# Performance work log

Measured on AMD Instinct MI355X. Metric: run time of the kernel, lower is better.

The kernel has to match this reference:

```python
import jax, jax.numpy as jnp
import numpy as np

D_MODEL = 512
N_HEADS = 8
D_HEAD = D_MODEL // N_HEADS
SCALE = D_HEAD ** -0.5


def _rel_shift(x):
    # x: (b, h, qlen, klen) -> Transformer-XL relative shift
    b, h, qlen, klen = x.shape
    x = jnp.pad(x, ((0, 0), (0, 0), (0, 0), (1, 0)))        # (b,h,q,k+1)
    x = x.reshape(b, h, klen + 1, qlen)
    x = x[:, :, 1:, :].reshape(b, h, qlen, klen)
    return x


def setup_inputs() -> dict:
    key = jax.random.key(0)
    ks = jax.random.split(key, 12)
    B, S = 2, 2048
    P = 2 * S - 1
    w = lambda k, shape: (jax.random.normal(k, shape, jnp.float32) * 0.02)
    return {
        "x": jax.random.normal(ks[0], (B, S, D_MODEL), jnp.float32),
        "pos_emb": jax.random.normal(ks[1], (P, D_MODEL), jnp.float32),
        "Wq": w(ks[2], (D_MODEL, D_MODEL)), "bq": jnp.zeros((D_MODEL,), jnp.float32),
        "Wk": w(ks[3], (D_MODEL, D_MODEL)), "bk": jnp.zeros((D_MODEL,), jnp.float32),
        "Wv": w(ks[4], (D_MODEL, D_MODEL)), "bv": jnp.zeros((D_MODEL,), jnp.float32),
        "Wp": w(ks[5], (D_MODEL, D_MODEL)),
        "Wo": w(ks[6], (D_MODEL, D_MODEL)), "bo": jnp.zeros((D_MODEL,), jnp.float32),
        "pos_bias_u": w(ks[7], (N_HEADS, D_HEAD)),
        "pos_bias_v": w(ks[8], (N_HEADS, D_HEAD)),
    }


def reference(x, pos_emb, Wq, bq, Wk, bk, Wv, bv, Wp, Wo, bo, pos_bias_u, pos_bias_v):
    B, S, _ = x.shape
    # projections (torch Linear: y = x @ W^T + b; here W stored as (in, out))
    q = (x @ Wq + bq).reshape(B, S, N_HEADS, D_HEAD)
    k = (x @ Wk + bk).reshape(B, S, N_HEADS, D_HEAD)
    v = (x @ Wv + bv).reshape(B, S, N_HEADS, D_HEAD)
    p = (pos_emb @ Wp).reshape(-1, N_HEADS, D_HEAD)  # (2S-1, H, D)

    # content score: (q + u) @ k^T  -> (B,H,S,S)
    content = jnp.einsum("bshd,bthd->bhst", q + pos_bias_u, k)
    # position score: (q + v_bias) @ p^T -> (B,H,S,2S-1), then rel_shift
    pos = jnp.einsum("bshd,phd->bhsp", q + pos_bias_v, p)
    pos = _rel_shift(pos)[..., :S]  # trim to kv_len

    attn = jax.nn.softmax((content + pos) * SCALE, axis=-1)
    out = jnp.einsum("bhst,bthd->bshd", attn, v).reshape(B, S, D_MODEL)
    out = out @ Wo + bo
    return out
```

## Files before the change

kernel.cpp:

```cpp
#include <hip/hip_runtime.h>

#define DM    512
#define NH    8
#define DH    64
#define SEQ   2048
#define PLEN  4095
#define NB    2
#define ATT_SCALE 0.125f

typedef __attribute__((ext_vector_type(8))) _Float16 half8;
typedef __attribute__((ext_vector_type(4))) float   floatx4;

__global__ __launch_bounds__(256)
void prep(const float* __restrict__ x, const float* __restrict__ pe,
          const float* __restrict__ W0, const float* __restrict__ W1,
          const float* __restrict__ W2, const float* __restrict__ W3,
          const float* __restrict__ W4,
          _Float16* __restrict__ x16, _Float16* __restrict__ pe16,
          _Float16* __restrict__ Wt)
{
    __shared__ _Float16 tile[64 * 72];
    const int z = blockIdx.z;
    const int t = threadIdx.x;

    if (z < 2) {
        const float* src = z ? pe : x;
        _Float16* dst = z ? pe16 : x16;
        const long n = z ? (long)PLEN * DM : (long)NB * SEQ * DM;
        const long i = ((long)blockIdx.x * 256 + t) * 8;
        if (i >= n) return;
        float4 f0 = *(const float4*)(src + i);
        float4 f1 = *(const float4*)(src + i + 4);
        half8 o;
        o[0] = (_Float16)f0.x; o[1] = (_Float16)f0.y;
        o[2] = (_Float16)f0.z; o[3] = (_Float16)f0.w;
        o[4] = (_Float16)f1.x; o[5] = (_Float16)f1.y;
        o[6] = (_Float16)f1.z; o[7] = (_Float16)f1.w;
        *(half8*)(dst + i) = o;
        return;
    }
    if (blockIdx.x >= 64) return;
    const int wz = z - 2;
    const float* W = (wz == 0) ? W0 : (wz == 1) ? W1 : (wz == 2) ? W2
                   : (wz == 3) ? W3 : W4;
    _Float16* dst_base = Wt + (size_t)wz * DM * DM;
    const int n0 = (blockIdx.x & 7) * 64, k0 = (blockIdx.x >> 3) * 64;
    {
        const int kr = t >> 2, nch = (t & 3) * 16;
        const float* src = W + (size_t)(k0 + kr) * DM + n0 + nch;
        float4 f0 = *(const float4*)(src + 0);
        float4 f1 = *(const float4*)(src + 4);
        float4 f2 = *(const float4*)(src + 8);
        float4 f3 = *(const float4*)(src + 12);
        _Float16* trow = &tile[kr * 72 + nch];
        trow[0]  = (_Float16)f0.x; trow[1]  = (_Float16)f0.y;
        trow[2]  = (_Float16)f0.z; trow[3]  = (_Float16)f0.w;
        trow[4]  = (_Float16)f1.x; trow[5]  = (_Float16)f1.y;
        trow[6]  = (_Float16)f1.z; trow[7]  = (_Float16)f1.w;
        trow[8]  = (_Float16)f2.x; trow[9]  = (_Float16)f2.y;
        trow[10] = (_Float16)f2.z; trow[11] = (_Float16)f2.w;
        trow[12] = (_Float16)f3.x; trow[13] = (_Float16)f3.y;
        trow[14] = (_Float16)f3.z; trow[15] = (_Float16)f3.w;
    }
    __syncthreads();
    {
        const int nr = t >> 2, kch = (t & 3) * 16;
        half8 o0, o1;
#pragma unroll
        for (int i = 0; i < 8; ++i) o0[i] = tile[(kch + i) * 72 + nr];
#pragma unroll
        for (int i = 0; i < 8; ++i) o1[i] = tile[(kch + 8 + i) * 72 + nr];
        _Float16* dst = dst_base + (size_t)(n0 + nr) * DM + k0 + kch;
        *(half8*)dst = o0;
        *(half8*)(dst + 8) = o1;
    }
}

__global__ __launch_bounds__(256)
void gemm_qkvp(const _Float16* __restrict__ X, const _Float16* __restrict__ Pe,
               const _Float16* __restrict__ Wt,
               const float* __restrict__ bq, const float* __restrict__ bk,
               const float* __restrict__ bv, const float* __restrict__ bu,
               const float* __restrict__ bvb,
               _Float16* __restrict__ qu16, _Float16* __restrict__ qv16,
               _Float16* __restrict__ k16, _Float16* __restrict__ vt16,
               _Float16* __restrict__ p16)
{
    __shared__ _Float16 aS[64 * 72];
    __shared__ _Float16 wS[64 * 72];

    const int t = threadIdx.x;
    const int w = t >> 6, lane = t & 63, quad = lane >> 4, l16 = lane & 15;
    const int z = blockIdx.z;
    const int n0 = blockIdx.x * 64;
    const int m0 = blockIdx.y * 64;
    const int srow = t >> 2, sch = (t & 3) * 16;
    const _Float16* A = (z == 3) ? Pe : X;
    const _Float16* Wz = Wt + (size_t)z * DM * DM;

    int arow = m0 + srow;
    if (z == 3 && arow > PLEN - 1) arow = PLEN - 1;
    const _Float16* arowp = A + (size_t)arow * DM + sch;
    const _Float16* wrowp = Wz + (size_t)(n0 + srow) * DM + sch;

    floatx4 acc[4];
#pragma unroll
    for (int ct = 0; ct < 4; ++ct) acc[ct] = (floatx4){0.f, 0.f, 0.f, 0.f};

    half8 pa0 = *(const half8*)arowp;
    half8 pa1 = *(const half8*)(arowp + 8);
    half8 pw0 = *(const half8*)wrowp;
    half8 pw1 = *(const half8*)(wrowp + 8);

    for (int k0 = 0; k0 < DM; k0 += 64) {
        __syncthreads();
        *(half8*)&aS[srow * 72 + sch]     = pa0;
        *(half8*)&aS[srow * 72 + sch + 8] = pa1;
        *(half8*)&wS[srow * 72 + sch]     = pw0;
        *(half8*)&wS[srow * 72 + sch + 8] = pw1;
        __syncthreads();
        if (k0 + 64 < DM) {
            pa0 = *(const half8*)(arowp + k0 + 64);
            pa1 = *(const half8*)(arowp + k0 + 72);
            pw0 = *(const half8*)(wrowp + k0 + 64);
            pw1 = *(const half8*)(wrowp + k0 + 72);
        }
#pragma unroll
        for (int kb = 0; kb < 2; ++kb) {
            half8 af = *(const half8*)&aS[(16 * w + l16) * 72 + kb * 32 + quad * 8];
#pragma unroll
            for (int ct = 0; ct < 4; ++ct) {
                half8 bf = *(const half8*)&wS[(16 * ct + l16) * 72 + kb * 32 + quad * 8];
                acc[ct] = __builtin_amdgcn_mfma_f32_16x16x32_f16(af, bf, acc[ct], 0, 0, 0);
            }
        }
    }

    const int h = n0 >> 6;
    if (z == 0) {
#pragma unroll
        for (int ct = 0; ct < 4; ++ct) {
            const int n = n0 + 16 * ct + l16;
            const float bval = bq[n], uval = bu[n], vval = bvb[n];
#pragma unroll
            for (int r = 0; r < 4; ++r) {
                const int m = m0 + 16 * w + 4 * quad + r;
                const int b = m >> 11, s = m & 2047;
                const size_t dst = ((size_t)((h * NB + b) * SEQ) + s) * DH + (n & 63);
                const float q = acc[ct][r] + bval;
                qu16[dst] = (_Float16)((q + uval) * ATT_SCALE);
                qv16[dst] = (_Float16)((q + vval) * ATT_SCALE);
            }
        }
    } else if (z == 1) {
#pragma unroll
        for (int ct = 0; ct < 4; ++ct) {
            const int n = n0 + 16 * ct + l16;
            const float bval = bk[n];
#pragma unroll
            for (int r = 0; r < 4; ++r) {
                const int m = m0 + 16 * w + 4 * quad + r;
                const int b = m >> 11, s = m & 2047;
                k16[((size_t)((h * NB + b) * SEQ) + s) * DH + (n & 63)] =
                    (_Float16)(acc[ct][r] + bval);
            }
        }
    } else if (z == 2) {
        __syncthreads();
#pragma unroll
        for (int ct = 0; ct < 4; ++ct) {
            const float bval = bv[n0 + 16 * ct + l16];
#pragma unroll
            for (int r = 0; r < 4; ++r)
                aS[(16 * w + 4 * quad + r) * 72 + 16 * ct + l16] =
                    (_Float16)(acc[ct][r] + bval);
        }
        __syncthreads();
        const int b = m0 >> 11, s0 = m0 & 2047;
        const int drow = t >> 2;
        half8 o0, o1;
#pragma unroll
        for (int i = 0; i < 8; ++i) o0[i] = aS[(sch + i) * 72 + drow];
#pragma unroll
        for (int i = 0; i < 8; ++i) o1[i] = aS[(sch + 8 + i) * 72 + drow];
        _Float16* dst = vt16 + ((size_t)((h * NB + b) * DH) + drow) * SEQ + s0 + sch;
        *(half8*)dst = o0;
        *(half8*)(dst + 8) = o1;
    } else {
#pragma unroll
        for (int ct = 0; ct < 4; ++ct) {
            const int n = n0 + 16 * ct + l16;
#pragma unroll
            for (int r = 0; r < 4; ++r) {
                const int m = m0 + 16 * w + 4 * quad + r;
                if (m < PLEN)
                    p16[((size_t)h * PLEN + m) * DH + (n & 63)] = (_Float16)acc[ct][r];
            }
        }
    }
}

__global__ __launch_bounds__(256, 2)
void relattn_mfma(const _Float16* __restrict__ QU,
                  const _Float16* __restrict__ QV,
                  const _Float16* __restrict__ Kp,
                  const _Float16* __restrict__ VT,
                  const _Float16* __restrict__ Pp,
                  _Float16* __restrict__ Out)
{
    __shared__ _Float16 kS[64 * 72];
    __shared__ _Float16 pS[128 * 72];
    __shared__ _Float16 vS[64 * 72];
    __shared__ _Float16 tS[64 * 88];

    const int t = threadIdx.x;
    const int w = t >> 6, lane = t & 63, quad = lane >> 4, l16 = lane & 15;
    const int i0 = blockIdx.x * 64;
    const int h = blockIdx.y, b = blockIdx.z;
    const size_t hb = (size_t)(h * NB + b);
    const int cbase = 48 - 16 * w;

    half8 qa[2], va[2];
    {
        const _Float16* qrow = QU + (hb * SEQ + i0 + 16 * w + l16) * DH + quad * 8;
        const _Float16* vrow = QV + (hb * SEQ + i0 + 16 * w + l16) * DH + quad * 8;
        qa[0] = *(const half8*)qrow;       qa[1] = *(const half8*)(qrow + 32);
        va[0] = *(const half8*)vrow;       va[1] = *(const half8*)(vrow + 32);
    }

    floatx4 O[4];
    float lsum[4] = {0.f, 0.f, 0.f, 0.f};
#pragma unroll
    for (int ct = 0; ct < 4; ++ct) O[ct] = (floatx4){0.f, 0.f, 0.f, 0.f};

    const int srow = t >> 2, schunk = (t & 3) * 16;
    const int prow = t >> 1, pch = (t & 1) * 32;

    const _Float16* Kbase = Kp + hb * SEQ * DH;
    const _Float16* Vbase = VT + hb * DH * SEQ;
    const _Float16* Pbase = Pp + (size_t)h * PLEN * DH;
    const int rbase0 = (SEQ - 1) - i0 - 63;

    half8 pk0, pk1, pv0, pv1;
    half8 pp0 = {}, pp1 = {}, pp2 = {}, pp3 = {};
    {
        const _Float16* src = Kbase + (size_t)srow * DH + schunk;
        pk0 = *(const half8*)src;
        pk1 = *(const half8*)(src + 8);
        const _Float16* vsrc = Vbase + (size_t)srow * SEQ + schunk;
        pv0 = *(const half8*)vsrc;
        pv1 = *(const half8*)(vsrc + 8);
        if (prow < 127) {
            const _Float16* psrc = Pbase + (size_t)(rbase0 + prow) * DH + pch;
            pp0 = *(const half8*)(psrc + 0);
            pp1 = *(const half8*)(psrc + 8);
            pp2 = *(const half8*)(psrc + 16);
            pp3 = *(const half8*)(psrc + 24);
        }
    }

    for (int j0 = 0; j0 < SEQ; j0 += 64) {
        __syncthreads();

        *(half8*)&kS[srow * 72 + schunk]     = pk0;
        *(half8*)&kS[srow * 72 + schunk + 8] = pk1;
        *(half8*)&vS[srow * 72 + schunk]     = pv0;
        *(half8*)&vS[srow * 72 + schunk + 8] = pv1;
        if (prow < 127) {
            *(half8*)&pS[prow * 72 + pch + 0]  = pp0;
            *(half8*)&pS[prow * 72 + pch + 8]  = pp1;
            *(half8*)&pS[prow * 72 + pch + 16] = pp2;
            *(half8*)&pS[prow * 72 + pch + 24] = pp3;
        }
        __syncthreads();

        if (j0 + 64 < SEQ) {
            const _Float16* src = Kbase + (size_t)(j0 + 64 + srow) * DH + schunk;
            pk0 = *(const half8*)src;
            pk1 = *(const half8*)(src + 8);
            const _Float16* vsrc = Vbase + (size_t)srow * SEQ + j0 + 64 + schunk;
            pv0 = *(const half8*)vsrc;
            pv1 = *(const half8*)(vsrc + 8);
            if (prow < 127) {
                const _Float16* psrc = Pbase + (size_t)(rbase0 + j0 + 64 + prow) * DH + pch;
                pp0 = *(const half8*)(psrc + 0);
                pp1 = *(const half8*)(psrc + 8);
                pp2 = *(const half8*)(psrc + 16);
                pp3 = *(const half8*)(psrc + 24);
            }
        }

        {
            floatx4 Tacc[5];
#pragma unroll
            for (int c2 = 0; c2 < 5; ++c2) Tacc[c2] = (floatx4){0.f, 0.f, 0.f, 0.f};
#pragma unroll
            for (int kb = 0; kb < 2; ++kb) {
#pragma unroll
                for (int c2 = 0; c2 < 5; ++c2) {
                    half8 bf = *(const half8*)&pS[(cbase + 16 * c2 + l16) * 72 + kb * 32 + quad * 8];
                    Tacc[c2] = __builtin_amdgcn_mfma_f32_16x16x32_f16(va[kb], bf, Tacc[c2], 0, 0, 0);
                }
            }
#pragma unroll
            for (int c2 = 0; c2 < 5; ++c2)
#pragma unroll
                for (int r = 0; r < 4; ++r)
                    tS[(16 * w + 4 * quad + r) * 88 + 16 * c2 + l16] = (_Float16)Tacc[c2][r];
        }
        asm volatile("" ::: "memory");

        floatx4 Sc[4];
#pragma unroll
        for (int ct = 0; ct < 4; ++ct) Sc[ct] = (floatx4){0.f, 0.f, 0.f, 0.f};
#pragma unroll
        for (int kb = 0; kb < 2; ++kb) {
#pragma unroll
            for (int ct = 0; ct < 4; ++ct) {
                half8 bf = *(const half8*)&kS[(16 * ct + l16) * 72 + kb * 32 + quad * 8];
                Sc[ct] = __builtin_amdgcn_mfma_f32_16x16x32_f16(qa[kb], bf, Sc[ct], 0, 0, 0);
            }
        }
#pragma unroll
        for (int ct = 0; ct < 4; ++ct)
#pragma unroll
            for (int r = 0; r < 4; ++r) {
                const int il16 = 4 * quad + r;
                const int c = 16 * ct + l16 - il16 + 15;
                const float e = __expf(Sc[ct][r] +
                                       (float)tS[(16 * w + il16) * 88 + c]);
                Sc[ct][r] = e;
                lsum[r] += e;
            }
        asm volatile("" ::: "memory");

#pragma unroll
        for (int ct = 0; ct < 4; ++ct)
#pragma unroll
            for (int r = 0; r < 4; ++r)
                tS[(16 * w + 4 * quad + r) * 88 + 16 * ct + l16] = (_Float16)Sc[ct][r];
        asm volatile("" ::: "memory");

#pragma unroll
        for (int kb = 0; kb < 2; ++kb) {
            half8 af = *(const half8*)&tS[(16 * w + l16) * 88 + kb * 32 + quad * 8];
#pragma unroll
            for (int ct = 0; ct < 4; ++ct) {
                half8 bf = *(const half8*)&vS[(16 * ct + l16) * 72 + kb * 32 + quad * 8];
                O[ct] = __builtin_amdgcn_mfma_f32_16x16x32_f16(af, bf, O[ct], 0, 0, 0);
            }
        }
        asm volatile("" ::: "memory");
    }

#pragma unroll
    for (int r = 0; r < 4; ++r) {
#pragma unroll
        for (int m = 1; m < 16; m <<= 1) lsum[r] += __shfl_xor(lsum[r], m);
        const float inv = 1.f / lsum[r];
        _Float16* orow = Out + (size_t)(b * SEQ + i0 + 16 * w + 4 * quad + r) * DM + h * DH;
#pragma unroll
        for (int ct = 0; ct < 4; ++ct)
            orow[16 * ct + l16] = (_Float16)(O[ct][r] * inv);
    }
}

__global__ __launch_bounds__(256)
void gemm_out(const _Float16* __restrict__ A, const _Float16* __restrict__ Wt,
              const float* __restrict__ bias, float* __restrict__ Out)
{
    __shared__ _Float16 aS[64 * 72];
    __shared__ _Float16 wS[64 * 72];

    const int t = threadIdx.x;
    const int w = t >> 6, lane = t & 63, quad = lane >> 4, l16 = lane & 15;
    const int n0 = blockIdx.x * 64;
    const int m0 = blockIdx.y * 64;
    const int srow = t >> 2, sch = (t & 3) * 16;

    const _Float16* arowp = A + (size_t)(m0 + srow) * DM + sch;
    const _Float16* wrowp = Wt + (size_t)(n0 + srow) * DM + sch;

    floatx4 acc[4];
#pragma unroll
    for (int ct = 0; ct < 4; ++ct) acc[ct] = (floatx4){0.f, 0.f, 0.f, 0.f};

    half8 pa0 = *(const half8*)arowp;
    half8 pa1 = *(const half8*)(arowp + 8);
    half8 pw0 = *(const half8*)wrowp;
    half8 pw1 = *(const half8*)(wrowp + 8);

    for (int k0 = 0; k0 < DM; k0 += 64) {
        __syncthreads();
        *(half8*)&aS[srow * 72 + sch]     = pa0;
        *(half8*)&aS[srow * 72 + sch + 8] = pa1;
        *(half8*)&wS[srow * 72 + sch]     = pw0;
        *(half8*)&wS[srow * 72 + sch + 8] = pw1;
        __syncthreads();
        if (k0 + 64 < DM) {
            pa0 = *(const half8*)(arowp + k0 + 64);
            pa1 = *(const half8*)(arowp + k0 + 72);
            pw0 = *(const half8*)(wrowp + k0 + 64);
            pw1 = *(const half8*)(wrowp + k0 + 72);
        }
#pragma unroll
        for (int kb = 0; kb < 2; ++kb) {
            half8 af = *(const half8*)&aS[(16 * w + l16) * 72 + kb * 32 + quad * 8];
#pragma unroll
            for (int ct = 0; ct < 4; ++ct) {
                half8 bf = *(const half8*)&wS[(16 * ct + l16) * 72 + kb * 32 + quad * 8];
                acc[ct] = __builtin_amdgcn_mfma_f32_16x16x32_f16(af, bf, acc[ct], 0, 0, 0);
            }
        }
    }

#pragma unroll
    for (int ct = 0; ct < 4; ++ct) {
        const int n = n0 + 16 * ct + l16;
        const float bval = bias[n];
#pragma unroll
        for (int r = 0; r < 4; ++r) {
            const int m = m0 + 16 * w + 4 * quad + r;
            Out[(size_t)m * DM + n] = acc[ct][r] + bval;
        }
    }
}

extern "C" void kernel_launch(void* const* d_in, const int* in_sizes, int n_in,
                              void* d_out, int out_size, void* d_ws, size_t ws_size,
                              hipStream_t stream)
{
    (void)in_sizes; (void)n_in; (void)out_size; (void)ws_size;
    const float* x   = (const float*)d_in[0];
    const float* pe  = (const float*)d_in[1];
    const float* Wq  = (const float*)d_in[2];
    const float* bq  = (const float*)d_in[3];
    const float* Wk  = (const float*)d_in[4];
    const float* bk  = (const float*)d_in[5];
    const float* Wv  = (const float*)d_in[6];
    const float* bv  = (const float*)d_in[7];
    const float* Wp  = (const float*)d_in[8];
    const float* Wo  = (const float*)d_in[9];
    const float* bo  = (const float*)d_in[10];
    const float* pbu = (const float*)d_in[11];
    const float* pbv = (const float*)d_in[12];
    float* out = (float*)d_out;

    const size_t nX  = (size_t)NB * SEQ * DM;
    const size_t nPe = (size_t)PLEN * DM;
    const size_t nW  = (size_t)DM * DM;
    const size_t nH  = (size_t)NH * NB * SEQ * DH;
    const size_t nPh = (size_t)NH * PLEN * DH;

    _Float16* x16  = (_Float16*)d_ws;
    _Float16* pe16 = x16 + nX;
    _Float16* wt   = pe16 + nPe;
    _Float16* qu16 = wt + 5 * nW;
    _Float16* qv16 = qu16 + nH;
    _Float16* k16  = qv16 + nH;
    _Float16* vt16 = k16 + nH;
    _Float16* p16  = vt16 + nH;
    _Float16* ow16 = p16 + nPh;

    dim3 blk(256);
    prep<<<dim3(1024, 1, 7), blk, 0, stream>>>(x, pe, Wq, Wk, Wv, Wp, Wo,
                                               x16, pe16, wt);
    gemm_qkvp<<<dim3(8, 64, 4), blk, 0, stream>>>(x16, pe16, wt,
                                                  bq, bk, bv, pbu, pbv,
                                                  qu16, qv16, k16, vt16, p16);
    relattn_mfma<<<dim3(SEQ / 64, NH, NB), blk, 0, stream>>>(
        qu16, qv16, k16, vt16, p16, ow16);
    gemm_out<<<dim3(8, 64), blk, 0, stream>>>(ow16, wt + 4 * nW, bo, out);
}
```

Before: 187.0 us.

## Fuse fp32-to-fp16 activation conversion into projection GEMM and repad score tile

Removes the separate pass that converts x and pos_emb to fp16 in the prep kernel. The QKVP GEMM now loads fp32 activations directly and converts them while staging into shared memory, saving a full write and re-read of the converted activations. The cost is that each GEMM block reads twice the bytes per A element, and those rows are re-read across the 8 column blocks. The shared score tile row pitch also changes from 88 to 84 halves, which alters the LDS bank access pattern.

After: 202.3 us. 1.08x slower.

```diff
diff --git a/kernel.cpp b/kernel.cpp
--- a/kernel.cpp
+++ b/kernel.cpp
@@ -7,40 +7,19 @@
 #define PLEN  4095
 #define NB    2
 #define ATT_SCALE 0.125f
+#define TP    84
 
 typedef __attribute__((ext_vector_type(8))) _Float16 half8;
 typedef __attribute__((ext_vector_type(4))) float   floatx4;
 
 __global__ __launch_bounds__(256)
-void prep(const float* __restrict__ x, const float* __restrict__ pe,
-          const float* __restrict__ W0, const float* __restrict__ W1,
+void prep(const float* __restrict__ W0, const float* __restrict__ W1,
           const float* __restrict__ W2, const float* __restrict__ W3,
-          const float* __restrict__ W4,
-          _Float16* __restrict__ x16, _Float16* __restrict__ pe16,
-          _Float16* __restrict__ Wt)
+          const float* __restrict__ W4, _Float16* __restrict__ Wt)
 {
     __shared__ _Float16 tile[64 * 72];
-    const int z = blockIdx.z;
     const int t = threadIdx.x;
-
-    if (z < 2) {
-        const float* src = z ? pe : x;
-        _Float16* dst = z ? pe16 : x16;
-        const long n = z ? (long)PLEN * DM : (long)NB * SEQ * DM;
-        const long i = ((long)blockIdx.x * 256 + t) * 8;
-        if (i >= n) return;
-        float4 f0 = *(const float4*)(src + i);
-        float4 f1 = *(const float4*)(src + i + 4);
-        half8 o;
-        o[0] = (_Float16)f0.x; o[1] = (_Float16)f0.y;
-        o[2] = (_Float16)f0.z; o[3] = (_Float16)f0.w;
-        o[4] = (_Float16)f1.x; o[5] = (_Float16)f1.y;
-        o[6] = (_Float16)f1.z; o[7] = (_Float16)f1.w;
-        *(half8*)(dst + i) = o;
-        return;
-    }
-    if (blockIdx.x >= 64) return;
-    const int wz = z - 2;
+    const int wz = blockIdx.z;
     const float* W = (wz == 0) ? W0 : (wz == 1) ? W1 : (wz == 2) ? W2
                    : (wz == 3) ? W3 : W4;
     _Float16* dst_base = Wt + (size_t)wz * DM * DM;
@@ -77,7 +56,7 @@
 }
 
 __global__ __launch_bounds__(256)
-void gemm_qkvp(const _Float16* __restrict__ X, const _Float16* __restrict__ Pe,
+void gemm_qkvp(const float* __restrict__ X, const float* __restrict__ Pe,
                const _Float16* __restrict__ Wt,
                const float* __restrict__ bq, const float* __restrict__ bk,
                const float* __restrict__ bv, const float* __restrict__ bu,
@@ -95,33 +74,48 @@
     const int n0 = blockIdx.x * 64;
     const int m0 = blockIdx.y * 64;
     const int srow = t >> 2, sch = (t & 3) * 16;
-    const _Float16* A = (z == 3) ? Pe : X;
+    const float* A = (z == 3) ? Pe : X;
     const _Float16* Wz = Wt + (size_t)z * DM * DM;
 
     int arow = m0 + srow;
     if (z == 3 && arow > PLEN - 1) arow = PLEN - 1;
-    const _Float16* arowp = A + (size_t)arow * DM + sch;
+    const float* arowp = A + (size_t)arow * DM + sch;
     const _Float16* wrowp = Wz + (size_t)(n0 + srow) * DM + sch;
 
     floatx4 acc[4];
 #pragma unroll
     for (int ct = 0; ct < 4; ++ct) acc[ct] = (floatx4){0.f, 0.f, 0.f, 0.f};
 
-    half8 pa0 = *(const half8*)arowp;
-    half8 pa1 = *(const half8*)(arowp + 8);
+    float4 pa0 = *(const float4*)(arowp + 0);
+    float4 pa1 = *(const float4*)(arowp + 4);
+    float4 pa2 = *(const float4*)(arowp + 8);
+    float4 pa3 = *(const float4*)(arowp + 12);
     half8 pw0 = *(const half8*)wrowp;
     half8 pw1 = *(const half8*)(wrowp + 8);
 
     for (int k0 = 0; k0 < DM; k0 += 64) {
         __syncthreads();
-        *(half8*)&aS[srow * 72 + sch]     = pa0;
-        *(half8*)&aS[srow * 72 + sch + 8] = pa1;
+        {
+            half8 h0, h1;
+            h0[0] = (_Float16)pa0.x; h0[1] = (_Float16)pa0.y;
+            h0[2] = (_Float16)pa0.z; h0[3] = (_Float16)pa0.w;
+            h0[4] = (_Float16)pa1.x; h0[5] = (_Float16)pa1.y;
+            h0[6] = (_Float16)pa1.z; h0[7] = (_Float16)pa1.w;
+            h1[0] = (_Float16)pa2.x; h1[1] = (_Float16)pa2.y;
+            h1[2] = (_Float16)pa2.z; h1[3] = (_Float16)pa2.w;
+            h1[4] = (_Float16)pa3.x; h1[5] = (_Float16)pa3.y;
+            h1[6] = (_Float16)pa3.z; h1[7] = (_Float16)pa3.w;
+            *(half8*)&aS[srow * 72 + sch]     = h0;
+            *(half8*)&aS[srow * 72 + sch + 8] = h1;
+        }
         *(half8*)&wS[srow * 72 + sch]     = pw0;
         *(half8*)&wS[srow * 72 + sch + 8] = pw1;
         __syncthreads();
         if (k0 + 64 < DM) {
-            pa0 = *(const half8*)(arowp + k0 + 64);
-            pa1 = *(const half8*)(arowp + k0 + 72);
+            pa0 = *(const float4*)(arowp + k0 + 64);
+            pa1 = *(const float4*)(arowp + k0 + 68);
+            pa2 = *(const float4*)(arowp + k0 + 72);
+            pa3 = *(const float4*)(arowp + k0 + 76);
             pw0 = *(const half8*)(wrowp + k0 + 64);
             pw1 = *(const half8*)(wrowp + k0 + 72);
         }
@@ -211,7 +205,7 @@
     __shared__ _Float16 kS[64 * 72];
     __shared__ _Float16 pS[128 * 72];
     __shared__ _Float16 vS[64 * 72];
-    __shared__ _Float16 tS[64 * 88];
+    __shared__ _Float16 tS[64 * TP];
 
     const int t = threadIdx.x;
     const int w = t >> 6, lane = t & 63, quad = lane >> 4, l16 = lane & 15;
@@ -306,7 +300,7 @@
             for (int c2 = 0; c2 < 5; ++c2)
 #pragma unroll
                 for (int r = 0; r < 4; ++r)
-                    tS[(16 * w + 4 * quad + r) * 88 + 16 * c2 + l16] = (_Float16)Tacc[c2][r];
+                    tS[(16 * w + 4 * quad + r) * TP + 16 * c2 + l16] = (_Float16)Tacc[c2][r];
         }
         asm volatile("" ::: "memory");
 
@@ -328,7 +322,7 @@
                 const int il16 = 4 * quad + r;
                 const int c = 16 * ct + l16 - il16 + 15;
                 const float e = __expf(Sc[ct][r] +
-                                       (float)tS[(16 * w + il16) * 88 + c]);
+                                       (float)tS[(16 * w + il16) * TP + c]);
                 Sc[ct][r] = e;
                 lsum[r] += e;
             }
@@ -338,12 +332,12 @@
         for (int ct = 0; ct < 4; ++ct)
 #pragma unroll
             for (int r = 0; r < 4; ++r)
-                tS[(16 * w + 4 * quad + r) * 88 + 16 * ct + l16] = (_Float16)Sc[ct][r];
+                tS[(16 * w + 4 * quad + r) * TP + 16 * ct + l16] = (_Float16)Sc[ct][r];
         asm volatile("" ::: "memory");
 
 #pragma unroll
         for (int kb = 0; kb < 2; ++kb) {
-            half8 af = *(const half8*)&tS[(16 * w + l16) * 88 + kb * 32 + quad * 8];
+            half8 af = *(const half8*)&tS[(16 * w + l16) * TP + kb * 32 + quad * 8];
 #pragma unroll
             for (int ct = 0; ct < 4; ++ct) {
                 half8 bf = *(const half8*)&vS[(16 * ct + l16) * 72 + kb * 32 + quad * 8];
@@ -446,15 +440,11 @@
     const float* pbv = (const float*)d_in[12];
     float* out = (float*)d_out;
 
-    const size_t nX  = (size_t)NB * SEQ * DM;
-    const size_t nPe = (size_t)PLEN * DM;
     const size_t nW  = (size_t)DM * DM;
     const size_t nH  = (size_t)NH * NB * SEQ * DH;
     const size_t nPh = (size_t)NH * PLEN * DH;
 
-    _Float16* x16  = (_Float16*)d_ws;
-    _Float16* pe16 = x16 + nX;
-    _Float16* wt   = pe16 + nPe;
+    _Float16* wt   = (_Float16*)d_ws;
     _Float16* qu16 = wt + 5 * nW;
     _Float16* qv16 = qu16 + nH;
     _Float16* k16  = qv16 + nH;
@@ -463,9 +453,8 @@
     _Float16* ow16 = p16 + nPh;
 
     dim3 blk(256);
-    prep<<<dim3(1024, 1, 7), blk, 0, stream>>>(x, pe, Wq, Wk, Wv, Wp, Wo,
-                                               x16, pe16, wt);
-    gemm_qkvp<<<dim3(8, 64, 4), blk, 0, stream>>>(x16, pe16, wt,
+    prep<<<dim3(64, 1, 5), blk, 0, stream>>>(Wq, Wk, Wv, Wp, Wo, wt);
+    gemm_qkvp<<<dim3(8, 64, 4), blk, 0, stream>>>(x, pe, wt,
                                                   bq, bk, bv, pbu, pbv,
                                                   qu16, qv16, k16, vt16, p16);
     relattn_mfma<<<dim3(SEQ / 64, NH, NB), blk, 0, stream>>>(
```
